# Optimization experiments

Measured on AMD Instinct MI355X. Metric: run time of the kernel, lower is better.

The kernel has to match this reference:

```python
import jax, jax.numpy as jnp
import numpy as np

N_ORDER = 256
BATCH = 512
SEQ_LEN = 4096


def make_legs_matrices(N):
    # HiPPO-LegS: A[n,k] = -sqrt(2n+1)sqrt(2k+1) for n>k, -(n+1) for n==k, 0 for n<k
    # B[n] = sqrt(2n+1)
    q = np.arange(N, dtype=np.float64)
    r = np.sqrt(2.0 * q + 1.0)
    M = r[:, None] * r[None, :] * (q[:, None] > q[None, :]).astype(np.float64)
    M = M + np.diag(q + 1.0)
    A = -M
    B = r[:, None]
    return jnp.asarray(A, jnp.float32), jnp.asarray(B, jnp.float32)


def setup_inputs() -> dict:
    key = jax.random.key(0)
    A, Bm = make_legs_matrices(N_ORDER)
    f = jax.random.normal(key, (BATCH, SEQ_LEN), dtype=jnp.float32)
    init_state = jnp.zeros((BATCH, 1, N_ORDER), dtype=jnp.float32)
    return {"f": f, "A": A, "Bm": Bm, "init_state": init_state}


def reference(f, A, Bm, init_state):
    # Generalized bilinear transform discretization, alpha = 0.5, step = 1.0
    step = 1.0
    alpha = 0.5
    N = A.shape[0]
    I = jnp.eye(N, dtype=A.dtype)
    inv_step = 1.0 / step
    part1 = I - inv_step * alpha * A
    part2 = I + inv_step * (1.0 - alpha) * A
    # Original uses lstsq; part1 is nonsingular so solve is equivalent.
    Ad = jnp.linalg.solve(part1, part2)            # (N, N)
    Bd = jnp.linalg.solve(part1, inv_step * Bm)    # (N, 1)

    BdT = Bd.T[None]  # (1, 1, N)

    def step_fn(c, f_k):
        # c: (B, 1, N), f_k: (B,)
        # c_k = c_{k-1} @ Ad^T + Bd^T * f_k
        c = jnp.einsum('bin,mn->bim', c, Ad) + BdT * f_k[:, None, None]
        return c, None

    # scan over time axis; batch fully vectorized inside each step
    c_k, _ = jax.lax.scan(step_fn, init_state, jnp.swapaxes(f, 0, 1))
    return c_k  # (B, 1, N)
```

## Files before the change

kernel.cpp:

```cpp
#include <hip/hip_runtime.h>

#define NORD 256
#define TLEN 4096
#define NBATCH 512

__global__ void inv_cols_kernel(const float* __restrict__ A,
                                const float* __restrict__ Bm,
                                float* __restrict__ P0,
                                float* __restrict__ U0) {
  const int col = blockIdx.x;
  const int i = threadIdx.x;
  const int wave = i >> 6;
  const int lane = i & 63;
  float b = (col < NORD) ? ((i == col) ? 1.0f : 0.0f) : Bm[i];
  const float invd = 1.0f / (1.0f - 0.5f * A[i * NORD + i]);
  __shared__ float xs[NORD];

  for (int w = 0; w < 4; ++w) {
    if (wave == w) {
      const int base = w << 6;
      for (int jj = 0; jj < 64; ++jj) {
        float bj = __shfl(b, jj);
        float dj = __shfl(invd, jj);
        float xj = bj * dj;
        if (lane > jj) {
          b += 0.5f * A[i * NORD + base + jj] * xj;
        } else if (lane == jj) {
          b = xj;
        }
      }
      xs[i] = b;
    }
    __syncthreads();
    if (wave > w) {
      const int base = w << 6;
      const float4* arow = reinterpret_cast<const float4*>(A + i * NORD + base);
#pragma unroll
      for (int q = 0; q < 16; ++q) {
        float4 a4 = arow[q];
        b += 0.5f * a4.x * xs[base + 4 * q + 0];
        b += 0.5f * a4.y * xs[base + 4 * q + 1];
        b += 0.5f * a4.z * xs[base + 4 * q + 2];
        b += 0.5f * a4.w * xs[base + 4 * q + 3];
      }
    }
  }
  if (col < NORD) {
    P0[i * NORD + col] = 2.0f * b - ((i == col) ? 1.0f : 0.0f);
  } else {
    U0[i] = b;
  }
}

__global__ void stage_kernel(const float* __restrict__ U_in,
                             float* __restrict__ U_out,
                             const float* __restrict__ P_in,
                             float* __restrict__ P_out,
                             int Jcount, int do_square) {
  const int t = threadIdx.x;
  const int tr = t >> 4, tc = t & 15;

  if (blockIdx.z == 1) {
    if (!do_square || blockIdx.x >= 8) return;
    __shared__ float At[32][33];
    __shared__ float Bt[32][33];
    const int m0 = blockIdx.x * 32, n0 = blockIdx.y * 32;
    float acc00 = 0.f, acc01 = 0.f, acc10 = 0.f, acc11 = 0.f;
    for (int k0 = 0; k0 < NORD; k0 += 32) {
      const int r = t >> 3, c4 = (t & 7) << 2;
      float4 va = *reinterpret_cast<const float4*>(&P_in[(m0 + r) * NORD + k0 + c4]);
      float4 vb = *reinterpret_cast<const float4*>(&P_in[(k0 + r) * NORD + n0 + c4]);
      At[r][c4] = va.x; At[r][c4 + 1] = va.y; At[r][c4 + 2] = va.z; At[r][c4 + 3] = va.w;
      Bt[r][c4] = vb.x; Bt[r][c4 + 1] = vb.y; Bt[r][c4 + 2] = vb.z; Bt[r][c4 + 3] = vb.w;
      __syncthreads();
#pragma unroll
      for (int k = 0; k < 32; ++k) {
        float a0 = At[tr][k], a1 = At[tr + 16][k];
        float b0 = Bt[k][tc], b1 = Bt[k][tc + 16];
        acc00 += a0 * b0; acc01 += a0 * b1;
        acc10 += a1 * b0; acc11 += a1 * b1;
      }
      __syncthreads();
    }
    P_out[(m0 + tr) * NORD + n0 + tc] = acc00;
    P_out[(m0 + tr) * NORD + n0 + tc + 16] = acc01;
    P_out[(m0 + tr + 16) * NORD + n0 + tc] = acc10;
    P_out[(m0 + tr + 16) * NORD + n0 + tc + 16] = acc11;
  } else {
    const int jb = blockIdx.x * 32;
    if (jb >= Jcount) return;
    __shared__ float Ut[32][33];
    __shared__ float Pt[32][33];
    const int m0 = blockIdx.y * 32;
    float acc00 = 0.f, acc01 = 0.f, acc10 = 0.f, acc11 = 0.f;
    for (int k0 = 0; k0 < NORD; k0 += 32) {
      const int r = t >> 3, c4 = (t & 7) << 2;
      const int j = jb + r;
      if (j < Jcount) {
        float4 vu = *reinterpret_cast<const float4*>(&U_in[j * NORD + k0 + c4]);
        Ut[r][c4] = vu.x; Ut[r][c4 + 1] = vu.y; Ut[r][c4 + 2] = vu.z; Ut[r][c4 + 3] = vu.w;
      } else {
        Ut[r][c4] = 0.f; Ut[r][c4 + 1] = 0.f; Ut[r][c4 + 2] = 0.f; Ut[r][c4 + 3] = 0.f;
      }
      float4 vp = *reinterpret_cast<const float4*>(&P_in[(m0 + r) * NORD + k0 + c4]);
      Pt[r][c4] = vp.x; Pt[r][c4 + 1] = vp.y; Pt[r][c4 + 2] = vp.z; Pt[r][c4 + 3] = vp.w;
      __syncthreads();
#pragma unroll
      for (int k = 0; k < 32; ++k) {
        float a0 = Ut[tr][k], a1 = Ut[tr + 16][k];
        float b0 = Pt[tc][k], b1 = Pt[tc + 16][k];
        acc00 += a0 * b0; acc01 += a0 * b1;
        acc10 += a1 * b0; acc11 += a1 * b1;
      }
      __syncthreads();
    }
    if (jb + tr < Jcount) {
      U_out[(jb + tr) * NORD + m0 + tc] = acc00;
      U_out[(jb + tr) * NORD + m0 + tc + 16] = acc01;
    }
    if (jb + tr + 16 < Jcount) {
      U_out[(jb + tr + 16) * NORD + m0 + tc] = acc10;
      U_out[(jb + tr + 16) * NORD + m0 + tc + 16] = acc11;
    }
  }
}

__global__ void final_gemm(const float* __restrict__ f,
                           const float* __restrict__ U,
                           float* __restrict__ C) {
  const int b0 = blockIdx.x * 64;
  const int m0 = blockIdx.y * 64;
  const int k0base = blockIdx.z * 512;
  __shared__ float At[64][17];
  __shared__ float Bt[16][65];
  const int t = threadIdx.x;
  const int tr = t >> 4, tc = t & 15;
  float acc[4][4] = {};
  for (int kc = 0; kc < 512; kc += 16) {
    const int k0 = k0base + kc;
    {
      const int r = t >> 2, c4 = (t & 3) << 2;
      float4 v = *reinterpret_cast<const float4*>(&f[(size_t)(b0 + r) * TLEN + k0 + c4]);
      At[r][c4] = v.x; At[r][c4 + 1] = v.y; At[r][c4 + 2] = v.z; At[r][c4 + 3] = v.w;
    }
    {
      const int r = t >> 4, c4 = (t & 15) << 2;
      float4 v = *reinterpret_cast<const float4*>(&U[(size_t)(TLEN - 1 - (k0 + r)) * NORD + m0 + c4]);
      Bt[r][c4] = v.x; Bt[r][c4 + 1] = v.y; Bt[r][c4 + 2] = v.z; Bt[r][c4 + 3] = v.w;
    }
    __syncthreads();
#pragma unroll
    for (int k = 0; k < 16; ++k) {
      float a[4], bb[4];
#pragma unroll
      for (int ii = 0; ii < 4; ++ii) a[ii] = At[tr + 16 * ii][k];
#pragma unroll
      for (int jj = 0; jj < 4; ++jj) bb[jj] = Bt[k][tc + 16 * jj];
#pragma unroll
      for (int ii = 0; ii < 4; ++ii)
#pragma unroll
        for (int jj = 0; jj < 4; ++jj)
          acc[ii][jj] += a[ii] * bb[jj];
    }
    __syncthreads();
  }
#pragma unroll
  for (int ii = 0; ii < 4; ++ii)
#pragma unroll
    for (int jj = 0; jj < 4; ++jj)
      atomicAdd(&C[(size_t)(b0 + tr + 16 * ii) * NORD + m0 + tc + 16 * jj], acc[ii][jj]);
}

extern "C" void kernel_launch(void* const* d_in, const int* in_sizes, int n_in,
                              void* d_out, int out_size, void* d_ws, size_t ws_size,
                              hipStream_t stream) {
  const float* f  = (const float*)d_in[0];
  const float* A  = (const float*)d_in[1];
  const float* Bm = (const float*)d_in[2];

  float* ws = (float*)d_ws;
  float* Pa = ws;
  float* Pb = ws + NORD * NORD;
  float* U  = ws + 2 * NORD * NORD;

  hipMemsetAsync(d_out, 0, (size_t)NBATCH * NORD * sizeof(float), stream);

  hipLaunchKernelGGL(inv_cols_kernel, dim3(NORD + 1), dim3(NORD), 0, stream,
                     A, Bm, Pa, U);

  for (int s = 0; s < 12; ++s) {
    const int J = 1 << s;
    const float* Pin = (s & 1) ? Pb : Pa;
    float* Pout = (s & 1) ? Pa : Pb;
    const int do_sq = (s < 11) ? 1 : 0;
    int jx = (J + 31) / 32;
    if (jx < 8) jx = 8;
    dim3 grid(jx, 8, do_sq ? 2 : 1);
    hipLaunchKernelGGL(stage_kernel, grid, dim3(256), 0, stream,
                       U, U + (size_t)J * NORD, Pin, Pout, J, do_sq);
  }

  hipLaunchKernelGGL(final_gemm, dim3(8, 4, 8), dim3(256), 0, stream,
                     f, U, (float*)d_out);
}
```

Baseline: 223.9 us.

## Fuse all stages into one persistent cooperative kernel with split-K and larger tiles

```diff
diff --git a/kernel.cpp b/kernel.cpp
--- a/kernel.cpp
+++ b/kernel.cpp
@@ -1,174 +1,246 @@
 #include <hip/hip_runtime.h>
+#include <hip/hip_cooperative_groups.h>
+
+namespace cg = cooperative_groups;
 
 #define NORD 256
 #define TLEN 4096
 #define NBATCH 512
-
-__global__ void inv_cols_kernel(const float* __restrict__ A,
-                                const float* __restrict__ Bm,
-                                float* __restrict__ P0,
-                                float* __restrict__ U0) {
-  const int col = blockIdx.x;
-  const int i = threadIdx.x;
-  const int wave = i >> 6;
-  const int lane = i & 63;
-  float b = (col < NORD) ? ((i == col) ? 1.0f : 0.0f) : Bm[i];
-  const float invd = 1.0f / (1.0f - 0.5f * A[i * NORD + i]);
-  __shared__ float xs[NORD];
-
-  for (int w = 0; w < 4; ++w) {
-    if (wave == w) {
-      const int base = w << 6;
-      for (int jj = 0; jj < 64; ++jj) {
-        float bj = __shfl(b, jj);
-        float dj = __shfl(invd, jj);
-        float xj = bj * dj;
-        if (lane > jj) {
-          b += 0.5f * A[i * NORD + base + jj] * xj;
-        } else if (lane == jj) {
-          b = xj;
-        }
-      }
-      xs[i] = b;
-    }
-    __syncthreads();
-    if (wave > w) {
-      const int base = w << 6;
-      const float4* arow = reinterpret_cast<const float4*>(A + i * NORD + base);
-#pragma unroll
-      for (int q = 0; q < 16; ++q) {
-        float4 a4 = arow[q];
-        b += 0.5f * a4.x * xs[base + 4 * q + 0];
-        b += 0.5f * a4.y * xs[base + 4 * q + 1];
-        b += 0.5f * a4.z * xs[base + 4 * q + 2];
-        b += 0.5f * a4.w * xs[base + 4 * q + 3];
-      }
-    }
-  }
-  if (col < NORD) {
-    P0[i * NORD + col] = 2.0f * b - ((i == col) ? 1.0f : 0.0f);
-  } else {
-    U0[i] = b;
-  }
-}
-
-__global__ void stage_kernel(const float* __restrict__ U_in,
-                             float* __restrict__ U_out,
-                             const float* __restrict__ P_in,
-                             float* __restrict__ P_out,
-                             int Jcount, int do_square) {
+#define NBLK 256
+#define NTHR 256
+
+__device__ __forceinline__ void fill_T2(float (*dst)[136], const float* __restrict__ s0,
+                                        const float* __restrict__ s1, int stride, int t) {
+  const int r = t & 63, qq = t >> 6;
+  const float* p0 = s0 + (size_t)r * stride + 4 * qq;
+  float4 v = *reinterpret_cast<const float4*>(p0);
+  float4 w = *reinterpret_cast<const float4*>(p0 + 16);
+  if (s1) {
+    const float* p1 = s1 + (size_t)r * stride + 4 * qq;
+    const float4 v1 = *reinterpret_cast<const float4*>(p1);
+    const float4 w1 = *reinterpret_cast<const float4*>(p1 + 16);
+    v.x += v1.x; v.y += v1.y; v.z += v1.z; v.w += v1.w;
+    w.x += w1.x; w.y += w1.y; w.z += w1.z; w.w += w1.w;
+  }
+  dst[4 * qq + 0][r] = v.x;  dst[4 * qq + 1][r] = v.y;
+  dst[4 * qq + 2][r] = v.z;  dst[4 * qq + 3][r] = v.w;
+  dst[4 * qq + 16][r] = w.x; dst[4 * qq + 17][r] = w.y;
+  dst[4 * qq + 18][r] = w.z; dst[4 * qq + 19][r] = w.w;
+}
+
+__device__ __forceinline__ void fill_N2(float (*dst)[136], const float* __restrict__ s0,
+                                        const float* __restrict__ s1, int stride, int t) {
+  const int kk = t >> 3, c8 = (t & 7) << 3;
+  const float* p0 = s0 + (size_t)kk * stride + c8;
+  float4 v = *reinterpret_cast<const float4*>(p0);
+  float4 w = *reinterpret_cast<const float4*>(p0 + 4);
+  if (s1) {
+    const float* p1 = s1 + (size_t)kk * stride + c8;
+    const float4 v1 = *reinterpret_cast<const float4*>(p1);
+    const float4 w1 = *reinterpret_cast<const float4*>(p1 + 4);
+    v.x += v1.x; v.y += v1.y; v.z += v1.z; v.w += v1.w;
+    w.x += w1.x; w.y += w1.y; w.z += w1.z; w.w += w1.w;
+  }
+  dst[kk][c8 + 0] = v.x; dst[kk][c8 + 1] = v.y; dst[kk][c8 + 2] = v.z; dst[kk][c8 + 3] = v.w;
+  dst[kk][c8 + 4] = w.x; dst[kk][c8 + 5] = w.y; dst[kk][c8 + 6] = w.z; dst[kk][c8 + 7] = w.w;
+}
+
+__device__ __forceinline__ void tile_fma4(const float (*As)[136], const float (*Bs)[136],
+                                          int tr, int tc, float acc[4][4]) {
+#pragma unroll
+  for (int k = 0; k < 32; ++k) {
+    const float4 a4 = *reinterpret_cast<const float4*>(&As[k][4 * tr]);
+    const float4 b4 = *reinterpret_cast<const float4*>(&Bs[k][4 * tc]);
+    const float a[4] = {a4.x, a4.y, a4.z, a4.w};
+    const float b[4] = {b4.x, b4.y, b4.z, b4.w};
+#pragma unroll
+    for (int ii = 0; ii < 4; ++ii)
+#pragma unroll
+      for (int jj = 0; jj < 4; ++jj)
+        acc[ii][jj] += a[ii] * b[jj];
+  }
+}
+
+__global__ __launch_bounds__(NTHR, 2) void hippo(
+    const float* __restrict__ A, const float* __restrict__ Bm,
+    const float* __restrict__ f,
+    float* P00, float* P01, float* P10, float* P11,
+    float* U0, float* U1,
+    float* C, int KS, int phase_lo, int phase_hi, int gs) {
+  cg::grid_group gg = cg::this_grid();
+  const int bid = blockIdx.x;
   const int t = threadIdx.x;
   const int tr = t >> 4, tc = t & 15;
 
-  if (blockIdx.z == 1) {
-    if (!do_square || blockIdx.x >= 8) return;
-    __shared__ float At[32][33];
-    __shared__ float Bt[32][33];
-    const int m0 = blockIdx.x * 32, n0 = blockIdx.y * 32;
-    float acc00 = 0.f, acc01 = 0.f, acc10 = 0.f, acc11 = 0.f;
-    for (int k0 = 0; k0 < NORD; k0 += 32) {
-      const int r = t >> 3, c4 = (t & 7) << 2;
-      float4 va = *reinterpret_cast<const float4*>(&P_in[(m0 + r) * NORD + k0 + c4]);
-      float4 vb = *reinterpret_cast<const float4*>(&P_in[(k0 + r) * NORD + n0 + c4]);
-      At[r][c4] = va.x; At[r][c4 + 1] = va.y; At[r][c4 + 2] = va.z; At[r][c4 + 3] = va.w;
-      Bt[r][c4] = vb.x; Bt[r][c4 + 1] = vb.y; Bt[r][c4 + 2] = vb.z; Bt[r][c4 + 3] = vb.w;
-      __syncthreads();
-#pragma unroll
-      for (int k = 0; k < 32; ++k) {
-        float a0 = At[tr][k], a1 = At[tr + 16][k];
-        float b0 = Bt[k][tc], b1 = Bt[k][tc + 16];
-        acc00 += a0 * b0; acc01 += a0 * b1;
-        acc10 += a1 * b0; acc11 += a1 * b1;
+  __shared__ float xs[NORD];
+  __shared__ float As[32][136];
+  __shared__ float Bs[32][136];
+
+  for (int ph = phase_lo; ph <= phase_hi; ++ph) {
+    if (ph == 0) {
+      for (int task = bid; task <= NORD; task += NBLK) {
+        __syncthreads();
+        const int i = t;
+        const int wave = i >> 6, lane = i & 63;
+        float b = (task < NORD) ? ((i == task) ? 1.0f : 0.0f) : Bm[i];
+        const float invd = 1.0f / (1.0f - 0.5f * A[i * NORD + i]);
+        for (int w = 0; w < 4; ++w) {
+          if (wave == w) {
+            const int base = w << 6;
+            for (int jj = 0; jj < 64; ++jj) {
+              float bj = __shfl(b, jj);
+              float dj = __shfl(invd, jj);
+              float xj = bj * dj;
+              if (lane > jj) {
+                b += 0.5f * A[i * NORD + base + jj] * xj;
+              } else if (lane == jj) {
+                b = xj;
+              }
+            }
+            xs[i] = b;
+          }
+          __syncthreads();
+          if (wave > w) {
+            const int base = w << 6;
+            const float4* arow = reinterpret_cast<const float4*>(A + i * NORD + base);
+#pragma unroll
+            for (int q = 0; q < 16; ++q) {
+              float4 a4 = arow[q];
+              b += 0.5f * (a4.x * xs[base + 4 * q + 0] + a4.y * xs[base + 4 * q + 1] +
+                           a4.z * xs[base + 4 * q + 2] + a4.w * xs[base + 4 * q + 3]);
+            }
+          }
+        }
+        if (task < NORD) {
+          P00[i * NORD + task] = 2.0f * b - ((i == task) ? 1.0f : 0.0f);
+        } else {
+          U0[i] = b;
+          if (U1) U1[i] = 0.0f;
+        }
       }
-      __syncthreads();
+      if (P01) P01[(size_t)bid * NTHR + t] = 0.0f;
+    } else if (ph <= 12) {
+      const int s = ph - 1;
+      const int J = 1 << s;
+      float* Pin0 = (s & 1) ? P10 : P00;
+      float* Pin1 = (s & 1) ? P11 : P01;
+      float* Pout0 = (s & 1) ? P00 : P10;
+      float* Pout1 = (s & 1) ? P01 : P11;
+      const int rtiles = (J + 63) >> 6;
+      const int n_apply = (rtiles << 2) * KS;
+      const int kspan = NORD / KS;
+
+      if (bid < n_apply) {
+        int work = bid, ks = 0;
+        if (KS == 2) { ks = work & 1; work >>= 1; }
+        const int j0 = (work >> 2) << 6;
+        const int m0 = (work & 3) << 6;
+        const int klo = ks * kspan;
+        float acc[4][4] = {};
+        for (int kc = 0; kc < kspan; kc += 32) {
+          const int k0 = klo + kc;
+          fill_T2(As, U0 + (size_t)j0 * NORD + k0,
+                  U1 ? U1 + (size_t)j0 * NORD + k0 : nullptr, NORD, t);
+          fill_T2(Bs, Pin0 + (size_t)m0 * NORD + k0,
+                  Pin1 ? Pin1 + (size_t)m0 * NORD + k0 : nullptr, NORD, t);
+          __syncthreads();
+          tile_fma4(As, Bs, tr, tc, acc);
+          __syncthreads();
+        }
+        float* Ud = ks ? U1 : U0;
+#pragma unroll
+        for (int ii = 0; ii < 4; ++ii) {
+          const int lr = j0 + 4 * tr + ii;
+          if (lr < J) {
+            float4 v = {acc[ii][0], acc[ii][1], acc[ii][2], acc[ii][3]};
+            *reinterpret_cast<float4*>(&Ud[(size_t)(J + lr) * NORD + m0 + 4 * tc]) = v;
+          }
+        }
+      } else if (s < 11 && bid < n_apply + 16 * KS) {
+        int q = bid - n_apply, ks = 0;
+        if (KS == 2) { ks = q & 1; q >>= 1; }
+        const int m0s = (q >> 2) << 6;
+        const int n0 = (q & 3) << 6;
+        const int klo = ks * kspan;
+        float acc[4][4] = {};
+        for (int kc = 0; kc < kspan; kc += 32) {
+          const int k0 = klo + kc;
+          fill_T2(As, Pin0 + (size_t)m0s * NORD + k0,
+                  Pin1 ? Pin1 + (size_t)m0s * NORD + k0 : nullptr, NORD, t);
+          fill_N2(Bs, Pin0 + (size_t)k0 * NORD + n0,
+                  Pin1 ? Pin1 + (size_t)k0 * NORD + n0 : nullptr, NORD, t);
+          __syncthreads();
+          tile_fma4(As, Bs, tr, tc, acc);
+          __syncthreads();
+        }
+        float* Pd = ks ? Pout1 : Pout0;
+#pragma unroll
+        for (int ii = 0; ii < 4; ++ii) {
+          float4 v = {acc[ii][0], acc[ii][1], acc[ii][2], acc[ii][3]};
+          *reinterpret_cast<float4*>(&Pd[(size_t)(m0s + 4 * tr + ii) * NORD + n0 + 4 * tc]) = v;
+        }
+      }
+    } else {
+      const int tile = bid & 7;
+      const int ksf = bid >> 3;
+      const int b0 = (tile >> 1) << 7;
+      const int m0 = (tile & 1) << 7;
+      const int k0b = ksf << 7;
+      const int r0 = (t >> 4) << 3, c0 = (t & 15) << 3;
+      float acc[8][8] = {};
+      for (int kc = 0; kc < 128; kc += 32) {
+        const int k0 = k0b + kc;
+        {
+          const int r = t >> 1, qb = (t & 1) << 4;
+          const float* p = f + (size_t)(b0 + r) * TLEN + k0 + qb;
+#pragma unroll
+          for (int j = 0; j < 4; ++j) {
+            float4 v = *reinterpret_cast<const float4*>(p + 4 * j);
+            As[qb + 4 * j + 0][r] = v.x; As[qb + 4 * j + 1][r] = v.y;
+            As[qb + 4 * j + 2][r] = v.z; As[qb + 4 * j + 3][r] = v.w;
+          }
+        }
+        {
+          const int kk = t >> 3, c16 = (t & 7) << 4;
+          const size_t row = (size_t)(TLEN - 1 - (k0 + kk)) * NORD + m0 + c16;
+          const float* p0 = U0 + row;
+          const float* p1 = U1 ? U1 + row : nullptr;
+#pragma unroll
+          for (int j = 0; j < 4; ++j) {
+            float4 v = *reinterpret_cast<const float4*>(p0 + 4 * j);
+            if (p1) {
+              const float4 w = *reinterpret_cast<const float4*>(p1 + 4 * j);
+              v.x += w.x; v.y += w.y; v.z += w.z; v.w += w.w;
+            }
+            Bs[kk][c16 + 4 * j + 0] = v.x; Bs[kk][c16 + 4 * j + 1] = v.y;
+            Bs[kk][c16 + 4 * j + 2] = v.z; Bs[kk][c16 + 4 * j + 3] = v.w;
+          }
+        }
+        __syncthreads();
+#pragma unroll
+        for (int k = 0; k < 32; ++k) {
+          const float4 a0 = *reinterpret_cast<const float4*>(&As[k][r0]);
+          const float4 a1 = *reinterpret_cast<const float4*>(&As[k][r0 + 4]);
+          const float4 b0v = *reinterpret_cast<const float4*>(&Bs[k][c0]);
+          const float4 b1v = *reinterpret_cast<const float4*>(&Bs[k][c0 + 4]);
+          const float a[8] = {a0.x, a0.y, a0.z, a0.w, a1.x, a1.y, a1.z, a1.w};
+          const float b[8] = {b0v.x, b0v.y, b0v.z, b0v.w, b1v.x, b1v.y, b1v.z, b1v.w};
+#pragma unroll
+          for (int ii = 0; ii < 8; ++ii)
+#pragma unroll
+            for (int jj = 0; jj < 8; ++jj)
+              acc[ii][jj] += a[ii] * b[jj];
+        }
+        __syncthreads();
+      }
+#pragma unroll
+      for (int ii = 0; ii < 8; ++ii)
+#pragma unroll
+        for (int jj = 0; jj < 8; ++jj)
+          atomicAdd(&C[(size_t)(b0 + r0 + ii) * NORD + m0 + c0 + jj], acc[ii][jj]);
     }
-    P_out[(m0 + tr) * NORD + n0 + tc] = acc00;
-    P_out[(m0 + tr) * NORD + n0 + tc + 16] = acc01;
-    P_out[(m0 + tr + 16) * NORD + n0 + tc] = acc10;
-    P_out[(m0 + tr + 16) * NORD + n0 + tc + 16] = acc11;
-  } else {
-    const int jb = blockIdx.x * 32;
-    if (jb >= Jcount) return;
-    __shared__ float Ut[32][33];
-    __shared__ float Pt[32][33];
-    const int m0 = blockIdx.y * 32;
-    float acc00 = 0.f, acc01 = 0.f, acc10 = 0.f, acc11 = 0.f;
-    for (int k0 = 0; k0 < NORD; k0 += 32) {
-      const int r = t >> 3, c4 = (t & 7) << 2;
-      const int j = jb + r;
-      if (j < Jcount) {
-        float4 vu = *reinterpret_cast<const float4*>(&U_in[j * NORD + k0 + c4]);
-        Ut[r][c4] = vu.x; Ut[r][c4 + 1] = vu.y; Ut[r][c4 + 2] = vu.z; Ut[r][c4 + 3] = vu.w;
-      } else {
-        Ut[r][c4] = 0.f; Ut[r][c4 + 1] = 0.f; Ut[r][c4 + 2] = 0.f; Ut[r][c4 + 3] = 0.f;
-      }
-      float4 vp = *reinterpret_cast<const float4*>(&P_in[(m0 + r) * NORD + k0 + c4]);
-      Pt[r][c4] = vp.x; Pt[r][c4 + 1] = vp.y; Pt[r][c4 + 2] = vp.z; Pt[r][c4 + 3] = vp.w;
-      __syncthreads();
-#pragma unroll
-      for (int k = 0; k < 32; ++k) {
-        float a0 = Ut[tr][k], a1 = Ut[tr + 16][k];
-        float b0 = Pt[tc][k], b1 = Pt[tc + 16][k];
-        acc00 += a0 * b0; acc01 += a0 * b1;
-        acc10 += a1 * b0; acc11 += a1 * b1;
-      }
-      __syncthreads();
-    }
-    if (jb + tr < Jcount) {
-      U_out[(jb + tr) * NORD + m0 + tc] = acc00;
-      U_out[(jb + tr) * NORD + m0 + tc + 16] = acc01;
-    }
-    if (jb + tr + 16 < Jcount) {
-      U_out[(jb + tr + 16) * NORD + m0 + tc] = acc10;
-      U_out[(jb + tr + 16) * NORD + m0 + tc + 16] = acc11;
-    }
-  }
-}
-
-__global__ void final_gemm(const float* __restrict__ f,
-                           const float* __restrict__ U,
-                           float* __restrict__ C) {
-  const int b0 = blockIdx.x * 64;
-  const int m0 = blockIdx.y * 64;
-  const int k0base = blockIdx.z * 512;
-  __shared__ float At[64][17];
-  __shared__ float Bt[16][65];
-  const int t = threadIdx.x;
-  const int tr = t >> 4, tc = t & 15;
-  float acc[4][4] = {};
-  for (int kc = 0; kc < 512; kc += 16) {
-    const int k0 = k0base + kc;
-    {
-      const int r = t >> 2, c4 = (t & 3) << 2;
-      float4 v = *reinterpret_cast<const float4*>(&f[(size_t)(b0 + r) * TLEN + k0 + c4]);
-      At[r][c4] = v.x; At[r][c4 + 1] = v.y; At[r][c4 + 2] = v.z; At[r][c4 + 3] = v.w;
-    }
-    {
-      const int r = t >> 4, c4 = (t & 15) << 2;
-      float4 v = *reinterpret_cast<const float4*>(&U[(size_t)(TLEN - 1 - (k0 + r)) * NORD + m0 + c4]);
-      Bt[r][c4] = v.x; Bt[r][c4 + 1] = v.y; Bt[r][c4 + 2] = v.z; Bt[r][c4 + 3] = v.w;
-    }
-    __syncthreads();
-#pragma unroll
-    for (int k = 0; k < 16; ++k) {
-      float a[4], bb[4];
-#pragma unroll
-      for (int ii = 0; ii < 4; ++ii) a[ii] = At[tr + 16 * ii][k];
-#pragma unroll
-      for (int jj = 0; jj < 4; ++jj) bb[jj] = Bt[k][tc + 16 * jj];
-#pragma unroll
-      for (int ii = 0; ii < 4; ++ii)
-#pragma unroll
-        for (int jj = 0; jj < 4; ++jj)
-          acc[ii][jj] += a[ii] * bb[jj];
-    }
-    __syncthreads();
-  }
-#pragma unroll
-  for (int ii = 0; ii < 4; ++ii)
-#pragma unroll
-    for (int jj = 0; jj < 4; ++jj)
-      atomicAdd(&C[(size_t)(b0 + tr + 16 * ii) * NORD + m0 + tc + 16 * jj], acc[ii][jj]);
+    if (gs && ph < phase_hi) gg.sync();
+  }
 }
 
 extern "C" void kernel_launch(void* const* d_in, const int* in_sizes, int n_in,
@@ -179,27 +251,34 @@
   const float* Bm = (const float*)d_in[2];
 
   float* ws = (float*)d_ws;
-  float* Pa = ws;
-  float* Pb = ws + NORD * NORD;
-  float* U  = ws + 2 * NORD * NORD;
+  const size_t need_split = (size_t)(4 * 65536 + 2 * 1048576) * sizeof(float);
+  int KS = (ws_size >= need_split) ? 2 : 1;
+
+  float *P00, *P01, *P10, *P11, *U0, *U1;
+  if (KS == 2) {
+    P00 = ws;            P01 = ws + 65536;
+    P10 = ws + 131072;   P11 = ws + 196608;
+    U0  = ws + 262144;   U1  = U0 + 1048576;
+  } else {
+    P00 = ws;            P01 = nullptr;
+    P10 = ws + 65536;    P11 = nullptr;
+    U0  = ws + 131072;   U1  = nullptr;
+  }
+  float* C = (float*)d_out;
 
   hipMemsetAsync(d_out, 0, (size_t)NBATCH * NORD * sizeof(float), stream);
 
-  hipLaunchKernelGGL(inv_cols_kernel, dim3(NORD + 1), dim3(NORD), 0, stream,
-                     A, Bm, Pa, U);
-
-  for (int s = 0; s < 12; ++s) {
-    const int J = 1 << s;
-    const float* Pin = (s & 1) ? Pb : Pa;
-    float* Pout = (s & 1) ? Pa : Pb;
-    const int do_sq = (s < 11) ? 1 : 0;
-    int jx = (J + 31) / 32;
-    if (jx < 8) jx = 8;
-    dim3 grid(jx, 8, do_sq ? 2 : 1);
-    hipLaunchKernelGGL(stage_kernel, grid, dim3(256), 0, stream,
-                       U, U + (size_t)J * NORD, Pin, Pout, J, do_sq);
-  }
-
-  hipLaunchKernelGGL(final_gemm, dim3(8, 4, 8), dim3(256), 0, stream,
-                     f, U, (float*)d_out);
-}
+  int pl = 0, phh = 13, gs = 1;
+  void* args[] = {(void*)&A, (void*)&Bm, (void*)&f,
+                  (void*)&P00, (void*)&P01, (void*)&P10, (void*)&P11,
+                  (void*)&U0, (void*)&U1, (void*)&C,
+                  (void*)&KS, (void*)&pl, (void*)&phh, (void*)&gs};
+  hipError_t e = hipLaunchCooperativeKernel((void*)hippo, dim3(NBLK), dim3(NTHR),
+                                            args, 0, stream);
+  if (e != hipSuccess) {
+    for (int p = 0; p <= 13; ++p) {
+      hipLaunchKernelGGL(hippo, dim3(NBLK), dim3(NTHR), 0, stream,
+                         A, Bm, f, P00, P01, P10, P11, U0, U1, C, KS, p, p, 0);
+    }
+  }
+}
```

After: 791.7 us. 3.54x slower.
